# Kernel optimization log

Measured on AMD Instinct MI355X. Metric: run time of the kernel, lower is better.

Reference implementation:

```python
import jax, jax.numpy as jnp
import numpy as np

B, T, H, W = 512, 8, 28, 28
VTH, VRESET = 1.0, 0.0
ALPHA = 2.0  # spikingjelly ATan surrogate default alpha


@jax.custom_vjp
def heaviside_atan(x):
    # forward: binary spike; backward: ATan surrogate gradient
    return (x >= 0).astype(x.dtype)

def _ha_fwd(x):
    return (x >= 0).astype(x.dtype), x

def _ha_bwd(x, g):
    return (g * (ALPHA / 2.0) / (1.0 + (jnp.pi / 2.0 * ALPHA * x) ** 2),)

heaviside_atan.defvjp(_ha_fwd, _ha_bwd)


def conv3x3(x, w):
    return jax.lax.conv_general_dilated(
        x, w, (1, 1), 'SAME', dimension_numbers=('NCHW', 'OIHW', 'NCHW'))


def maxpool2(x):
    return jax.lax.reduce_window(x, -jnp.inf, jax.lax.max,
                                 (1, 1, 2, 2), (1, 1, 2, 2), 'VALID')


def one_spike_if(v, fired, x):
    # OneSpikeIFNode: integrate, fire at most once (fired mask), hard reset
    v = v + x
    spike = heaviside_atan(v - VTH) * (1.0 - fired)
    v = v * (1.0 - spike) + VRESET * spike
    fired = jnp.maximum(fired, jax.lax.stop_gradient(spike))
    return v, fired, spike


def if_node(v, x):
    # readout IFNode: integrate, fire, hard reset (v_threshold finite: latency mode, no warmup)
    v = v + x
    spike = heaviside_atan(v - VTH)
    v = v * (1.0 - spike) + VRESET * spike
    return v, spike


def setup_inputs() -> dict:
    key = jax.random.key(0)
    k = jax.random.split(key, 5)
    x = jax.random.uniform(k[0], (B, 1, H, W), jnp.float32)
    # weight scale (default_T / T) == 1 since T == 8 == default_T
    w_sconv = jax.random.normal(k[1], (16, 1, 3, 3), jnp.float32) * (2.0 / 3.0)
    w_conv = jax.random.normal(k[2], (16, 16, 3, 3), jnp.float32) * 0.12
    w_fc1 = jax.random.normal(k[3], (100, 16 * 14 * 14), jnp.float32) * 0.02
    w_fc2 = jax.random.normal(k[4], (10, 100), jnp.float32) * 0.15
    return {"x": x, "w_sconv": w_sconv, "w_conv": w_conv, "w_fc1": w_fc1, "w_fc2": w_fc2}


def reference(x, w_sconv, w_conv, w_fc1, w_fc2):
    xs = conv3x3(x, w_sconv)  # static conv computed once, reused every timestep
    z = jnp.zeros_like(xs)                       # [B,16,28,28]
    zp = jnp.zeros((B, 16, 14, 14), xs.dtype)    # pool fired-window mask
    zf = jnp.zeros((B, 100), xs.dtype)
    zo = jnp.zeros((B, 10), xs.dtype)
    state0 = (z, z, z, z, zp, zf, zf, zo)

    def step(state, _):
        v1, f1, v2, f2, pf, vfc, ffc, vout = state
        v1, f1, s1 = one_spike_if(v1, f1, xs)
        c = conv3x3(s1, w_conv)
        v2, f2, s2 = one_spike_if(v2, f2, c)
        # FirstSpikePool2d: max-pool spikes, each window passes only its first spike
        pooled = maxpool2(s2) * (1.0 - pf)
        pf = jnp.maximum(pf, jax.lax.stop_gradient(pooled))
        h = pooled.reshape(B, -1) @ w_fc1.T      # [B,100]
        vfc, ffc, s3 = one_spike_if(vfc, ffc, h)
        o = s3 @ w_fc2.T                          # [B,10]
        vout, s4 = if_node(vout, o)
        fr = jnp.stack([s1.mean(), s2.mean(), s3.mean(), s4.mean()])
        return (v1, f1, v2, f2, pf, vfc, ffc, vout), (s4, vout, fr)

    _, (s4_t, vout_t, fr_t) = jax.lax.scan(step, state0, None, length=T)
    counter_t = jnp.cumsum(s4_t, axis=0)                        # [T,B,10]
    latency_score = heaviside_atan(counter_t - 0.5).sum(axis=0)  # ATan_binary surrogate
    reg_loss = fr_t.max(axis=0).sum()
    return latency_score / T, reg_loss
```

## Files before the change

### kernel.cpp

```cpp
#include <hip/hip_runtime.h>

#define TB 512
#define NIMG 512
#define HW 28
#define NPIX 784
#define TT 8
#define NFC 100
#define NOUT 10
#define MAGIC 0x5C5C5C5Cu

#define WT_FLOATS 313600
#define GLB_ADD(p, v) __hip_atomic_fetch_add((p), (v), __ATOMIC_RELAXED, __HIP_MEMORY_SCOPE_AGENT)

typedef float f4 __attribute__((ext_vector_type(4)));

__global__ __launch_bounds__(TB, 4)
void snn_main(const float* __restrict__ xg, const float* __restrict__ w_sconv,
              const float* __restrict__ w_conv, const float* __restrict__ w_fc1,
              const float* __restrict__ w_fc2, float* __restrict__ wT,
              float* __restrict__ out, unsigned int* __restrict__ ctrl)
{
    __shared__ float wc[2880];
    __shared__ unsigned char spanB[25600];
    __shared__ unsigned short rowOr[TT * HW];
    __shared__ unsigned char tqA[3136];
    __shared__ unsigned short slist[3136];
    __shared__ float xst[NPIX];
    __shared__ float wsc[144];
    __shared__ int bcnt[9], bofs[9], bput[8];
    __shared__ int hist[32];
    __shared__ int lastflag;

    unsigned short* mask_t = (unsigned short*)spanB;
    unsigned int* mask32 = (unsigned int*)spanB;
    unsigned int* t2n = (unsigned int*)(spanB + 12544);
    float* prefixLDS = (float*)spanB;

    unsigned int* tflags = ctrl;
    float* fr_g = (float*)(ctrl + 98);
    unsigned int* done2 = ctrl + 130;
    unsigned int* fr_ready = ctrl + 131;

    const int tid = threadIdx.x;
    const int b = blockIdx.x;

    if (b < 98) {
        const int c0 = b * 32;
        for (int idx = tid; idx < 3200; idx += TB) {
            int c = idx / 100, r = idx - 100 * c;
            wT[(c0 + c) * 100 + r] = w_fc1[r * 3136 + c0 + c];
        }
    }
    if (b == 0 && tid < 33) ctrl[98 + tid] = 0u;

    for (int i = tid; i < NPIX; i += TB) xst[i] = xg[b * NPIX + i];
    for (int i = tid; i < 144; i += TB) wsc[i] = w_sconv[i];
    for (int i = tid; i < 2304; i += TB) {
        int c = i & 15, r = i >> 4;
        wc[r * 20 + c] = w_conv[c * 144 + r];
    }
    for (int i = tid; i < 3136; i += TB) mask32[i] = 0u;
    if (tid < 32) hist[tid] = 0;
    if (tid < 9) bcnt[tid] = 0;
    if (b < 98) __threadfence();
    __syncthreads();
    if (b < 98 && tid == 0) {
        __hip_atomic_store(&tflags[b], MAGIC, __ATOMIC_RELEASE, __HIP_MEMORY_SCOPE_AGENT);
        if (b == 0)
            __hip_atomic_store(fr_ready, MAGIC, __ATOMIC_RELEASE, __HIP_MEMORY_SCOPE_AGENT);
    }

    unsigned int pca = 0, pcb = 0;
#pragma unroll 1
    for (int e = 0; e < 25; e++) {
        int g = e * TB + tid;
        if (g < 12544) {
            int ci = g & 15, pos = g >> 4;
            int yy = pos / HW, xx = pos % HW;
            float acc = 0.f;
#pragma unroll
            for (int ky = 0; ky < 3; ky++) {
                int ys = yy + ky - 1;
                if (ys < 0 || ys >= HW) continue;
#pragma unroll
                for (int kx = 0; kx < 3; kx++) {
                    int xsrc = xx + kx - 1;
                    if (xsrc < 0 || xsrc >= HW) continue;
                    acc = fmaf(wsc[ci * 9 + ky * 3 + kx], xst[ys * HW + xsrc], acc);
                }
            }
            int t1 = 8; float v = 0.f;
#pragma unroll
            for (int t = 0; t < TT; t++) {
                v += acc;
                if (t1 == 8 && v >= 1.0f) t1 = t;
            }
            if (t1 < 8) {
                int lin = t1 * NPIX + pos;
                atomicOr(&mask32[lin >> 1], (1u << ci) << ((lin & 1) * 16));
                if (t1 < 4) pca += 1u << (t1 * 8); else pcb += 1u << ((t1 - 4) * 8);
            }
        }
    }
#pragma unroll
    for (int t = 0; t < TT; t++) {
        unsigned int c = ((t < 4 ? (pca >> (t * 8)) : (pcb >> ((t - 4) * 8))) & 255u);
        if (c) atomicAdd(&hist[t], (int)c);
    }
    __syncthreads();

    for (int i = tid; i < TT * HW; i += TB) {
        const unsigned short* mr = mask_t + (i / HW) * NPIX + (i % HW) * HW;
        unsigned int o = 0;
#pragma unroll
        for (int x = 0; x < HW; x++) o |= mr[x];
        rowOr[i] = (unsigned short)o;
    }
    __syncthreads();

    unsigned int pc2a = 0, pc2b = 0;
#pragma unroll 1
    for (int own = 0; own < 2; own++) {
        int pos = own * TB + tid;
        if (pos < NPIX) {
            int py = pos / HW, px = pos - py * HW;
            f4 vv0 = {0.f, 0.f, 0.f, 0.f}, vv1 = vv0, vv2 = vv0, vv3 = vv0;
            unsigned int done = 0;
            unsigned int t2lo = 0x88888888u, t2hi = 0x88888888u;
#pragma unroll 1
            for (int t = 0; t < TT; t++) {
                const unsigned short* ro = rowOr + t * HW;
                unsigned int un = ro[py];
                if (py > 0) un |= ro[py - 1];
                if (py < HW - 1) un |= ro[py + 1];
                if (!un) continue;
                const unsigned short* mt = mask_t + t * NPIX;
#pragma unroll
                for (int k = 0; k < 9; k++) {
                    int qy = py + k / 3 - 1, qx = px + k % 3 - 1;
                    if ((unsigned)qy >= HW || (unsigned)qx >= HW) continue;
                    unsigned int m = mt[qy * HW + qx];
                    while (m) {
                        int ci = __builtin_ctz(m); m &= m - 1;
                        const f4* wrow = (const f4*)&wc[(ci * 9 + k) * 20];
                        vv0 += wrow[0]; vv1 += wrow[1];
                        vv2 += wrow[2]; vv3 += wrow[3];
                    }
                }
                unsigned int fired = 0;
#pragma unroll
                for (int c = 0; c < 16; c++) {
                    float val = (c < 4) ? vv0[c & 3] : (c < 8) ? vv1[c & 3]
                              : (c < 12) ? vv2[c & 3] : vv3[c & 3];
                    fired |= (val >= 1.0f) ? (1u << c) : 0u;
                }
                unsigned int newf = fired & ~done;
                done |= newf;
                if (newf) {
                    int cnt = __builtin_popcount(newf);
                    if (t < 4) pc2a += (unsigned)cnt << (t * 8);
                    else       pc2b += (unsigned)cnt << ((t - 4) * 8);
                    while (newf) {
                        int c = __builtin_ctz(newf); newf &= newf - 1;
                        if (c < 8) t2lo = (t2lo & ~(15u << (4 * c))) | ((unsigned)t << (4 * c));
                        else       t2hi = (t2hi & ~(15u << (4 * (c - 8)))) | ((unsigned)t << (4 * (c - 8)));
                    }
                }
                if (done == 0xffffu) break;
            }
            t2n[pos * 2] = t2lo;
            t2n[pos * 2 + 1] = t2hi;
        }
    }
#pragma unroll
    for (int t = 0; t < TT; t++) {
        unsigned int c = ((t < 4 ? (pc2a >> (t * 8)) : (pc2b >> ((t - 4) * 8))) & 255u);
        if (c) atomicAdd(&hist[8 + t], (int)c);
    }
    __syncthreads();

    for (int u = tid; u < 3136; u += TB) {
        int c = u / 196, rem = u - c * 196;
        int wy = rem / 14, wx = rem - wy * 14;
        int p0 = wy * 56 + wx * 2;
        int wsel = c >> 3, sh = (c & 7) * 4;
        int m0 = (t2n[p0 * 2 + wsel] >> sh) & 15;
        int m1 = (t2n[(p0 + 1) * 2 + wsel] >> sh) & 15;
        int m2 = (t2n[(p0 + HW) * 2 + wsel] >> sh) & 15;
        int m3 = (t2n[(p0 + HW + 1) * 2 + wsel] >> sh) & 15;
        int tqv = min(min(m0, m1), min(m2, m3));
        tqA[u] = (unsigned char)tqv;
        if (tqv < 8) atomicAdd(&bcnt[tqv], 1);
    }
    __syncthreads();
    if (tid == 0) {
        int s = 0;
#pragma unroll
        for (int t = 0; t < TT; t++) { bofs[t] = s; s += bcnt[t]; }
        bofs[8] = s;
    }
    __syncthreads();
    if (tid < 8) bput[tid] = bofs[tid];
    __syncthreads();
    for (int u = tid; u < 3136; u += TB) {
        int tqv = tqA[u];
        if (tqv < 8) { int j = atomicAdd(&bput[tqv], 1); slist[j] = (unsigned short)u; }
    }

    if (tid < 98) {
        while (__hip_atomic_load(&tflags[tid], __ATOMIC_ACQUIRE,
                                 __HIP_MEMORY_SCOPE_AGENT) != MAGIC)
            __builtin_amdgcn_s_sleep(2);
    }
    __syncthreads();

    {
        const int lane = tid & 63;
        const int w = tid >> 6;
        const float* wA = wT + lane;
        const float* wB = wT + 64 + lane;
        float acc0 = 0.f, acc1 = 0.f;
#pragma unroll 1
        for (int t = 0; t < TT; t++) {
            const int lo = bofs[t];
            const int n = bofs[t + 1] - lo;
            int j = w;
            for (; j + 24 < n; j += 32) {
                int u0 = (int)slist[lo + j] * 100;
                int u1 = (int)slist[lo + j + 8] * 100;
                int u2 = (int)slist[lo + j + 16] * 100;
                int u3 = (int)slist[lo + j + 24] * 100;
                float a0 = wA[u0], a1 = wA[u1], a2 = wA[u2], a3 = wA[u3];
                if (lane < 36) {
                    float b0 = wB[u0], b1 = wB[u1], b2 = wB[u2], b3 = wB[u3];
                    acc1 += b0; acc1 += b1; acc1 += b2; acc1 += b3;
                }
                acc0 += a0; acc0 += a1; acc0 += a2; acc0 += a3;
            }
            for (; j < n; j += 8) {
                int u0 = (int)slist[lo + j] * 100;
                acc0 += wA[u0];
                if (lane < 36) acc1 += wB[u0];
            }
            prefixLDS[(w * TT + t) * NFC + lane] = acc0;
            if (lane < 36) prefixLDS[(w * TT + t) * NFC + 64 + lane] = acc1;
        }
    }
    __syncthreads();

    if (tid < NFC) {
        int t3 = 8;
#pragma unroll
        for (int t = 0; t < TT; t++) {
            float v = 0.f;
#pragma unroll
            for (int w = 0; w < 8; w++) v += prefixLDS[(w * TT + t) * NFC + tid];
            if (t3 == 8 && v >= 1.0f) t3 = t;
        }
        tqA[tid] = (unsigned char)t3;
        if (t3 < 8) atomicAdd(&hist[16 + t3], 1);
    }
    __syncthreads();

    if (tid < NOUT) {
        float acc8[TT] = {0.f, 0.f, 0.f, 0.f, 0.f, 0.f, 0.f, 0.f};
        for (int i = 0; i < NFC; i++) {
            float w = w_fc2[tid * NFC + i];
            int tv = tqA[i];
#pragma unroll
            for (int k = 0; k < TT; k++) acc8[k] += (tv == k) ? w : 0.f;
        }
        float vout = 0.f; int cnt = 0; float lat = 0.f;
#pragma unroll
        for (int t = 0; t < TT; t++) {
            vout += acc8[t];
            if (vout >= 1.0f) { vout = 0.f; cnt++; atomicAdd(&hist[24 + t], 1); }
            if (cnt >= 1) lat += 1.f;
        }
        out[b * NOUT + tid] = lat * 0.125f;
    }
    __syncthreads();

    if (tid == 0) {
        while (__hip_atomic_load(fr_ready, __ATOMIC_ACQUIRE,
                                 __HIP_MEMORY_SCOPE_AGENT) != MAGIC)
            __builtin_amdgcn_s_sleep(2);
    }
    __syncthreads();
    if (tid < 32) {
        int h = hist[tid];
        if (h) GLB_ADD(&fr_g[(tid & 7) * 4 + (tid >> 3)], (float)h);
    }
    __syncthreads();

    if (tid == 0) {
        unsigned int old = __hip_atomic_fetch_add(done2, 1u, __ATOMIC_ACQ_REL,
                                                  __HIP_MEMORY_SCOPE_AGENT);
        lastflag = (old == (unsigned)(NIMG - 1));
    }
    __syncthreads();
    if (lastflag && tid == 0) {
        const float inv0 = 1.f / 6422528.f;
        const float inv2 = 1.f / 51200.f;
        const float inv3 = 1.f / 5120.f;
        const float invs[4] = { inv0, inv0, inv2, inv3 };
        float reg = 0.f;
        for (int l = 0; l < 4; l++) {
            float mx = -INFINITY;
            for (int t = 0; t < TT; t++) {
                float v = __hip_atomic_load(&fr_g[t * 4 + l], __ATOMIC_RELAXED,
                                            __HIP_MEMORY_SCOPE_AGENT);
                mx = fmaxf(mx, v * invs[l]);
            }
            reg += mx;
        }
        out[NIMG * NOUT] = reg;
    }
}

extern "C" void kernel_launch(void* const* d_in, const int* in_sizes, int n_in,
                              void* d_out, int out_size, void* d_ws, size_t ws_size,
                              hipStream_t stream) {
    const float* x       = (const float*)d_in[0];
    const float* w_sconv = (const float*)d_in[1];
    const float* w_conv  = (const float*)d_in[2];
    const float* w_fc1   = (const float*)d_in[3];
    const float* w_fc2   = (const float*)d_in[4];
    float* out = (float*)d_out;

    float* wT          = (float*)d_ws;
    unsigned int* ctrl = (unsigned int*)(wT + WT_FLOATS);

    snn_main<<<NIMG, TB, 0, stream>>>(x, w_sconv, w_conv, w_fc1, w_fc2, wT,
                                      out, ctrl);
}
```

Measured before the change: 199.3 us.

## Split each image across two blocks by row halves with global FC1 partial merge

Each image is now processed by two blocks, each owning 14 output rows with a one-row halo for the spiking conv stages, halving per-block LDS and work. Per-half FC1 membrane partial sums are written to a global buffer, and the second block to finish (via a per-image atomic pair counter) combines them and runs the FC1 threshold, FC2 and output stages. Launch bounds rise to 8 waves-per-EU-class occupancy to exploit the smaller LDS footprint. This adds halo recomputation, extra global traffic and atomics, and cross-block synchronization in exchange for more parallelism across the GPU.

Measured after the change: 405.7 us. 2.04x slower.

```diff
diff --git a/kernel.cpp b/kernel.cpp
--- a/kernel.cpp
+++ b/kernel.cpp
@@ -10,48 +10,55 @@
 #define MAGIC 0x5C5C5C5Cu
 
 #define WT_FLOATS 313600
+#define VFCB_FLOATS (NIMG * 2 * TT * NFC)
 #define GLB_ADD(p, v) __hip_atomic_fetch_add((p), (v), __ATOMIC_RELAXED, __HIP_MEMORY_SCOPE_AGENT)
 
 typedef float f4 __attribute__((ext_vector_type(4)));
 
-__global__ __launch_bounds__(TB, 4)
+__global__ __launch_bounds__(TB, 8)
 void snn_main(const float* __restrict__ xg, const float* __restrict__ w_sconv,
               const float* __restrict__ w_conv, const float* __restrict__ w_fc1,
               const float* __restrict__ w_fc2, float* __restrict__ wT,
-              float* __restrict__ out, unsigned int* __restrict__ ctrl)
+              float* __restrict__ vfcb, float* __restrict__ out,
+              unsigned int* __restrict__ ctrl)
 {
-    __shared__ float wc[2880];
-    __shared__ unsigned char spanB[25600];
-    __shared__ unsigned short rowOr[TT * HW];
-    __shared__ unsigned char tqA[3136];
-    __shared__ unsigned short slist[3136];
-    __shared__ float xst[NPIX];
-    __shared__ float wsc[144];
+    __shared__ unsigned char span[25600] __attribute__((aligned(16)));
+    __shared__ unsigned short slist[1568];
+    __shared__ unsigned char tqA[1568];
     __shared__ int bcnt[9], bofs[9], bput[8];
     __shared__ int hist[32];
-    __shared__ int lastflag;
-
-    unsigned short* mask_t = (unsigned short*)spanB;
-    unsigned int* mask32 = (unsigned int*)spanB;
-    unsigned int* t2n = (unsigned int*)(spanB + 12544);
-    float* prefixLDS = (float*)spanB;
+    __shared__ int winflag, lastflag;
+
+    float* wc = (float*)span;
+    float* xst = (float*)(span + 11520);
+    unsigned int* t2n = (unsigned int*)(span + 11520);
+    float* wsc = (float*)(span + 14656);
+    unsigned short* mask_t = (unsigned short*)(span + 15232);
+    unsigned int* mask32 = (unsigned int*)(span + 15232);
+    unsigned short* rowOr = (unsigned short*)(span + 21952);
+    float* prefixLDS = (float*)span;
 
     unsigned int* tflags = ctrl;
     float* fr_g = (float*)(ctrl + 98);
     unsigned int* done2 = ctrl + 130;
     unsigned int* fr_ready = ctrl + 131;
+    unsigned int* pair = ctrl + 132;
 
     const int tid = threadIdx.x;
-    const int b = blockIdx.x;
-
-    if (b < 98) {
-        const int c0 = b * 32;
+    const int b = blockIdx.x >> 1;
+    const int half = blockIdx.x & 1;
+    const int mrow0 = half ? 13 : 0;
+
+    if (blockIdx.x < 98) {
+        const int c0 = blockIdx.x * 32;
         for (int idx = tid; idx < 3200; idx += TB) {
             int c = idx / 100, r = idx - 100 * c;
             wT[(c0 + c) * 100 + r] = w_fc1[r * 3136 + c0 + c];
         }
     }
-    if (b == 0 && tid < 33) ctrl[98 + tid] = 0u;
+    if (blockIdx.x == 0) {
+        for (int i = 98 + tid; i < 644; i += TB) ctrl[i] = 0u;
+    }
 
     for (int i = tid; i < NPIX; i += TB) xst[i] = xg[b * NPIX + i];
     for (int i = tid; i < 144; i += TB) wsc[i] = w_sconv[i];
@@ -59,28 +66,32 @@
         int c = i & 15, r = i >> 4;
         wc[r * 20 + c] = w_conv[c * 144 + r];
     }
-    for (int i = tid; i < 3136; i += TB) mask32[i] = 0u;
+    for (int i = tid; i < 1680; i += TB) mask32[i] = 0u;
     if (tid < 32) hist[tid] = 0;
     if (tid < 9) bcnt[tid] = 0;
-    if (b < 98) __threadfence();
-    __syncthreads();
-    if (b < 98 && tid == 0) {
-        __hip_atomic_store(&tflags[b], MAGIC, __ATOMIC_RELEASE, __HIP_MEMORY_SCOPE_AGENT);
-        if (b == 0)
-            __hip_atomic_store(fr_ready, MAGIC, __ATOMIC_RELEASE, __HIP_MEMORY_SCOPE_AGENT);
+    if (blockIdx.x < 98) __threadfence();
+    __syncthreads();
+    if (tid == 0) {
+        if (blockIdx.x < 98)
+            __hip_atomic_store(&tflags[blockIdx.x], MAGIC, __ATOMIC_RELEASE,
+                               __HIP_MEMORY_SCOPE_AGENT);
+        if (blockIdx.x == 0)
+            __hip_atomic_store(fr_ready, MAGIC, __ATOMIC_RELEASE,
+                               __HIP_MEMORY_SCOPE_AGENT);
     }
 
     unsigned int pca = 0, pcb = 0;
 #pragma unroll 1
-    for (int e = 0; e < 25; e++) {
+    for (int e = 0; e < 14; e++) {
         int g = e * TB + tid;
-        if (g < 12544) {
-            int ci = g & 15, pos = g >> 4;
-            int yy = pos / HW, xx = pos % HW;
+        if (g < 6720) {
+            int ci = g & 15, p = g >> 4;
+            int rl = p / HW, xx = p - rl * HW;
+            int gy = mrow0 + rl;
             float acc = 0.f;
 #pragma unroll
             for (int ky = 0; ky < 3; ky++) {
-                int ys = yy + ky - 1;
+                int ys = gy + ky - 1;
                 if (ys < 0 || ys >= HW) continue;
 #pragma unroll
                 for (int kx = 0; kx < 3; kx++) {
@@ -96,9 +107,12 @@
                 if (t1 == 8 && v >= 1.0f) t1 = t;
             }
             if (t1 < 8) {
-                int lin = t1 * NPIX + pos;
+                int lin = t1 * 420 + p;
                 atomicOr(&mask32[lin >> 1], (1u << ci) << ((lin & 1) * 16));
-                if (t1 < 4) pca += 1u << (t1 * 8); else pcb += 1u << ((t1 - 4) * 8);
+                bool owned = half ? (rl >= 1) : (rl < 14);
+                if (owned) {
+                    if (t1 < 4) pca += 1u << (t1 * 8); else pcb += 1u << ((t1 - 4) * 8);
+                }
             }
         }
     }
@@ -109,68 +123,66 @@
     }
     __syncthreads();
 
-    for (int i = tid; i < TT * HW; i += TB) {
-        const unsigned short* mr = mask_t + (i / HW) * NPIX + (i % HW) * HW;
+    for (int i = tid; i < TT * 15; i += TB) {
+        int t = i / 15, rl = i - t * 15;
+        const unsigned short* mr = mask_t + t * 420 + rl * HW;
         unsigned int o = 0;
 #pragma unroll
         for (int x = 0; x < HW; x++) o |= mr[x];
-        rowOr[i] = (unsigned short)o;
+        rowOr[t * 16 + rl] = (unsigned short)o;
     }
     __syncthreads();
 
     unsigned int pc2a = 0, pc2b = 0;
+    if (tid < 392) {
+        const int py_l = tid / HW, px = tid - py_l * HW;
+        const int cr = py_l + (half ? 1 : 0);
+        f4 vv0 = {0.f, 0.f, 0.f, 0.f}, vv1 = vv0, vv2 = vv0, vv3 = vv0;
+        unsigned int done = 0;
+        unsigned int t2lo = 0x88888888u, t2hi = 0x88888888u;
 #pragma unroll 1
-    for (int own = 0; own < 2; own++) {
-        int pos = own * TB + tid;
-        if (pos < NPIX) {
-            int py = pos / HW, px = pos - py * HW;
-            f4 vv0 = {0.f, 0.f, 0.f, 0.f}, vv1 = vv0, vv2 = vv0, vv3 = vv0;
-            unsigned int done = 0;
-            unsigned int t2lo = 0x88888888u, t2hi = 0x88888888u;
-#pragma unroll 1
-            for (int t = 0; t < TT; t++) {
-                const unsigned short* ro = rowOr + t * HW;
-                unsigned int un = ro[py];
-                if (py > 0) un |= ro[py - 1];
-                if (py < HW - 1) un |= ro[py + 1];
-                if (!un) continue;
-                const unsigned short* mt = mask_t + t * NPIX;
-#pragma unroll
-                for (int k = 0; k < 9; k++) {
-                    int qy = py + k / 3 - 1, qx = px + k % 3 - 1;
-                    if ((unsigned)qy >= HW || (unsigned)qx >= HW) continue;
-                    unsigned int m = mt[qy * HW + qx];
-                    while (m) {
-                        int ci = __builtin_ctz(m); m &= m - 1;
-                        const f4* wrow = (const f4*)&wc[(ci * 9 + k) * 20];
-                        vv0 += wrow[0]; vv1 += wrow[1];
-                        vv2 += wrow[2]; vv3 += wrow[3];
-                    }
-                }
-                unsigned int fired = 0;
-#pragma unroll
-                for (int c = 0; c < 16; c++) {
-                    float val = (c < 4) ? vv0[c & 3] : (c < 8) ? vv1[c & 3]
-                              : (c < 12) ? vv2[c & 3] : vv3[c & 3];
-                    fired |= (val >= 1.0f) ? (1u << c) : 0u;
-                }
-                unsigned int newf = fired & ~done;
-                done |= newf;
-                if (newf) {
-                    int cnt = __builtin_popcount(newf);
-                    if (t < 4) pc2a += (unsigned)cnt << (t * 8);
-                    else       pc2b += (unsigned)cnt << ((t - 4) * 8);
-                    while (newf) {
-                        int c = __builtin_ctz(newf); newf &= newf - 1;
-                        if (c < 8) t2lo = (t2lo & ~(15u << (4 * c))) | ((unsigned)t << (4 * c));
-                        else       t2hi = (t2hi & ~(15u << (4 * (c - 8)))) | ((unsigned)t << (4 * (c - 8)));
-                    }
-                }
-                if (done == 0xffffu) break;
-            }
-            t2n[pos * 2] = t2lo;
-            t2n[pos * 2 + 1] = t2hi;
-        }
+        for (int t = 0; t < TT; t++) {
+            const unsigned short* ro = rowOr + t * 16;
+            unsigned int un = ro[cr];
+            if (cr > 0) un |= ro[cr - 1];
+            if (cr < 14) un |= ro[cr + 1];
+            if (!un) continue;
+            const unsigned short* mt = mask_t + t * 420;
+#pragma unroll
+            for (int k = 0; k < 9; k++) {
+                int mr = cr + k / 3 - 1, qx = px + k % 3 - 1;
+                if ((unsigned)mr >= 15u || (unsigned)qx >= HW) continue;
+                unsigned int m = mt[mr * HW + qx];
+                while (m) {
+                    int ci = __builtin_ctz(m); m &= m - 1;
+                    const f4* wrow = (const f4*)&wc[(ci * 9 + k) * 20];
+                    vv0 += wrow[0]; vv1 += wrow[1];
+                    vv2 += wrow[2]; vv3 += wrow[3];
+                }
+            }
+            unsigned int fired = 0;
+#pragma unroll
+            for (int c = 0; c < 16; c++) {
+                float val = (c < 4) ? vv0[c & 3] : (c < 8) ? vv1[c & 3]
+                          : (c < 12) ? vv2[c & 3] : vv3[c & 3];
+                fired |= (val >= 1.0f) ? (1u << c) : 0u;
+            }
+            unsigned int newf = fired & ~done;
+            done |= newf;
+            if (newf) {
+                int cnt = __builtin_popcount(newf);
+                if (t < 4) pc2a += (unsigned)cnt << (t * 8);
+                else       pc2b += (unsigned)cnt << ((t - 4) * 8);
+                while (newf) {
+                    int c = __builtin_ctz(newf); newf &= newf - 1;
+                    if (c < 8) t2lo = (t2lo & ~(15u << (4 * c))) | ((unsigned)t << (4 * c));
+                    else       t2hi = (t2hi & ~(15u << (4 * (c - 8)))) | ((unsigned)t << (4 * (c - 8)));
+                }
+            }
+            if (done == 0xffffu) break;
+        }
+        t2n[tid * 2] = t2lo;
+        t2n[tid * 2 + 1] = t2hi;
     }
 #pragma unroll
     for (int t = 0; t < TT; t++) {
@@ -179,8 +191,8 @@
     }
     __syncthreads();
 
-    for (int u = tid; u < 3136; u += TB) {
-        int c = u / 196, rem = u - c * 196;
+    for (int u = tid; u < 1568; u += TB) {
+        int c = u / 98, rem = u - c * 98;
         int wy = rem / 14, wx = rem - wy * 14;
         int p0 = wy * 56 + wx * 2;
         int wsel = c >> 3, sh = (c & 7) * 4;
@@ -202,9 +214,14 @@
     __syncthreads();
     if (tid < 8) bput[tid] = bofs[tid];
     __syncthreads();
-    for (int u = tid; u < 3136; u += TB) {
+    for (int u = tid; u < 1568; u += TB) {
         int tqv = tqA[u];
-        if (tqv < 8) { int j = atomicAdd(&bput[tqv], 1); slist[j] = (unsigned short)u; }
+        if (tqv < 8) {
+            int j = atomicAdd(&bput[tqv], 1);
+            int c = u / 98, rem = u - c * 98;
+            int wy = rem / 14, wx = rem - wy * 14;
+            slist[j] = (unsigned short)(c * 196 + (half * 7 + wy) * 14 + wx);
+        }
     }
 
     if (tid < 98) {
@@ -249,12 +266,43 @@
     __syncthreads();
 
     if (tid < NFC) {
+#pragma unroll
+        for (int t = 0; t < TT; t++) {
+            float s = 0.f;
+#pragma unroll
+            for (int w = 0; w < 8; w++) s += prefixLDS[(w * TT + t) * NFC + tid];
+            vfcb[(((size_t)b * 2 + half) * TT + t) * NFC + tid] = s;
+        }
+    }
+
+    if (tid == 0) {
+        while (__hip_atomic_load(fr_ready, __ATOMIC_ACQUIRE,
+                                 __HIP_MEMORY_SCOPE_AGENT) != MAGIC)
+            __builtin_amdgcn_s_sleep(2);
+    }
+    __syncthreads();
+    if (tid < 16) {
+        int h = hist[tid];
+        if (h) GLB_ADD(&fr_g[(tid & 7) * 4 + (tid >> 3)], (float)h);
+    }
+    __threadfence();
+    __syncthreads();
+    if (tid == 0) {
+        unsigned int old = __hip_atomic_fetch_add(&pair[b], 1u, __ATOMIC_ACQ_REL,
+                                                  __HIP_MEMORY_SCOPE_AGENT);
+        winflag = (old == 1u);
+    }
+    __syncthreads();
+    if (!winflag) return;
+
+    if (tid < NFC) {
         int t3 = 8;
 #pragma unroll
         for (int t = 0; t < TT; t++) {
-            float v = 0.f;
-#pragma unroll
-            for (int w = 0; w < 8; w++) v += prefixLDS[(w * TT + t) * NFC + tid];
+            float v = __hip_atomic_load(&vfcb[(((size_t)b * 2 + 0) * TT + t) * NFC + tid],
+                                        __ATOMIC_RELAXED, __HIP_MEMORY_SCOPE_AGENT)
+                    + __hip_atomic_load(&vfcb[(((size_t)b * 2 + 1) * TT + t) * NFC + tid],
+                                        __ATOMIC_RELAXED, __HIP_MEMORY_SCOPE_AGENT);
             if (t3 == 8 && v >= 1.0f) t3 = t;
         }
         tqA[tid] = (unsigned char)t3;
@@ -280,17 +328,11 @@
         out[b * NOUT + tid] = lat * 0.125f;
     }
     __syncthreads();
-
-    if (tid == 0) {
-        while (__hip_atomic_load(fr_ready, __ATOMIC_ACQUIRE,
-                                 __HIP_MEMORY_SCOPE_AGENT) != MAGIC)
-            __builtin_amdgcn_s_sleep(2);
-    }
-    __syncthreads();
-    if (tid < 32) {
+    if (tid >= 16 && tid < 32) {
         int h = hist[tid];
         if (h) GLB_ADD(&fr_g[(tid & 7) * 4 + (tid >> 3)], (float)h);
     }
+    __threadfence();
     __syncthreads();
 
     if (tid == 0) {
@@ -329,8 +371,9 @@
     float* out = (float*)d_out;
 
     float* wT          = (float*)d_ws;
-    unsigned int* ctrl = (unsigned int*)(wT + WT_FLOATS);
-
-    snn_main<<<NIMG, TB, 0, stream>>>(x, w_sconv, w_conv, w_fc1, w_fc2, wT,
-                                      out, ctrl);
+    float* vfcb        = wT + WT_FLOATS;
+    unsigned int* ctrl = (unsigned int*)(vfcb + VFCB_FLOATS);
+
+    snn_main<<<NIMG * 2, TB, 0, stream>>>(x, w_sconv, w_conv, w_fc1, w_fc2,
+                                          wT, vfcb, out, ctrl);
 }
```

## Split each image across two blocks by output channel half, add readout kernel

Applied to the files above, without the earlier changes.

Each image is now handled by two blocks, each owning 8 of the 16 conv2 output channels. Both blocks recompute the first conv and spike mask, then write partial fc1 prefix sums to a global buffer. A second small kernel sums the two halves, runs the fc1 and readout spiking logic, and accumulates the firing-rate stats. The aim is more parallelism and a smaller LDS footprint for higher occupancy, at the cost of duplicated stage-1 work, an extra launch and a global round trip.

Result: slower. 207.7 us (+4.2%).

```diff
diff --git a/kernel.cpp b/kernel.cpp
--- a/kernel.cpp
+++ b/kernel.cpp
@@ -10,6 +10,7 @@
 #define MAGIC 0x5C5C5C5Cu
 
 #define WT_FLOATS 313600
+#define VFCB_FLOATS (NIMG * 2 * TT * NFC)
 #define GLB_ADD(p, v) __hip_atomic_fetch_add((p), (v), __ATOMIC_RELAXED, __HIP_MEMORY_SCOPE_AGENT)
 
 typedef float f4 __attribute__((ext_vector_type(4)));
@@ -18,56 +19,62 @@
 void snn_main(const float* __restrict__ xg, const float* __restrict__ w_sconv,
               const float* __restrict__ w_conv, const float* __restrict__ w_fc1,
               const float* __restrict__ w_fc2, float* __restrict__ wT,
-              float* __restrict__ out, unsigned int* __restrict__ ctrl)
+              float* __restrict__ vfcb, float* __restrict__ out,
+              unsigned int* __restrict__ ctrl)
 {
-    __shared__ float wc[2880];
-    __shared__ unsigned char spanB[25600];
-    __shared__ unsigned short rowOr[TT * HW];
-    __shared__ unsigned char tqA[3136];
-    __shared__ unsigned short slist[3136];
-    __shared__ float xst[NPIX];
-    __shared__ float wsc[144];
+    __shared__ unsigned char span[25600] __attribute__((aligned(16)));
+    __shared__ unsigned short slist[1568];
+    __shared__ unsigned char tqA[1568];
     __shared__ int bcnt[9], bofs[9], bput[8];
     __shared__ int hist[32];
-    __shared__ int lastflag;
-
-    unsigned short* mask_t = (unsigned short*)spanB;
-    unsigned int* mask32 = (unsigned int*)spanB;
-    unsigned int* t2n = (unsigned int*)(spanB + 12544);
-    float* prefixLDS = (float*)spanB;
+
+    float* wc = (float*)span;
+    float* xst = (float*)(span + 6912);
+    unsigned int* t2n = (unsigned int*)(span + 6912);
+    float* wsc = (float*)(span + 10048);
+    unsigned short* mask_t = (unsigned short*)(span + 10624);
+    unsigned int* mask32 = (unsigned int*)(span + 10624);
+    unsigned short* rowOr = (unsigned short*)(span + 23168);
+    float* prefixLDS = (float*)span;
 
     unsigned int* tflags = ctrl;
     float* fr_g = (float*)(ctrl + 98);
-    unsigned int* done2 = ctrl + 130;
     unsigned int* fr_ready = ctrl + 131;
 
     const int tid = threadIdx.x;
-    const int b = blockIdx.x;
-
-    if (b < 98) {
-        const int c0 = b * 32;
+    const int b = blockIdx.x >> 1;
+    const int half = blockIdx.x & 1;
+    const int co0 = half * 8;
+
+    if (blockIdx.x < 98) {
+        const int c0 = blockIdx.x * 32;
         for (int idx = tid; idx < 3200; idx += TB) {
             int c = idx / 100, r = idx - 100 * c;
             wT[(c0 + c) * 100 + r] = w_fc1[r * 3136 + c0 + c];
         }
     }
-    if (b == 0 && tid < 33) ctrl[98 + tid] = 0u;
+    if (blockIdx.x == 0) {
+        for (int i = 98 + tid; i < 132; i += TB) ctrl[i] = 0u;
+    }
 
     for (int i = tid; i < NPIX; i += TB) xst[i] = xg[b * NPIX + i];
     for (int i = tid; i < 144; i += TB) wsc[i] = w_sconv[i];
-    for (int i = tid; i < 2304; i += TB) {
-        int c = i & 15, r = i >> 4;
-        wc[r * 20 + c] = w_conv[c * 144 + r];
+    for (int i = tid; i < 1152; i += TB) {
+        int c = i & 7, r = i >> 3;
+        wc[r * 12 + c] = w_conv[(co0 + c) * 144 + r];
     }
     for (int i = tid; i < 3136; i += TB) mask32[i] = 0u;
     if (tid < 32) hist[tid] = 0;
     if (tid < 9) bcnt[tid] = 0;
-    if (b < 98) __threadfence();
-    __syncthreads();
-    if (b < 98 && tid == 0) {
-        __hip_atomic_store(&tflags[b], MAGIC, __ATOMIC_RELEASE, __HIP_MEMORY_SCOPE_AGENT);
-        if (b == 0)
-            __hip_atomic_store(fr_ready, MAGIC, __ATOMIC_RELEASE, __HIP_MEMORY_SCOPE_AGENT);
+    if (blockIdx.x < 98) __threadfence();
+    __syncthreads();
+    if (tid == 0) {
+        if (blockIdx.x < 98)
+            __hip_atomic_store(&tflags[blockIdx.x], MAGIC, __ATOMIC_RELEASE,
+                               __HIP_MEMORY_SCOPE_AGENT);
+        if (blockIdx.x == 0)
+            __hip_atomic_store(fr_ready, MAGIC, __ATOMIC_RELEASE,
+                               __HIP_MEMORY_SCOPE_AGENT);
     }
 
     unsigned int pca = 0, pcb = 0;
@@ -102,19 +109,22 @@
             }
         }
     }
-#pragma unroll
-    for (int t = 0; t < TT; t++) {
-        unsigned int c = ((t < 4 ? (pca >> (t * 8)) : (pcb >> ((t - 4) * 8))) & 255u);
-        if (c) atomicAdd(&hist[t], (int)c);
+    if (half == 0) {
+#pragma unroll
+        for (int t = 0; t < TT; t++) {
+            unsigned int c = ((t < 4 ? (pca >> (t * 8)) : (pcb >> ((t - 4) * 8))) & 255u);
+            if (c) atomicAdd(&hist[t], (int)c);
+        }
     }
     __syncthreads();
 
     for (int i = tid; i < TT * HW; i += TB) {
-        const unsigned short* mr = mask_t + (i / HW) * NPIX + (i % HW) * HW;
+        int t = i / HW, y = i - t * HW;
+        const unsigned short* mr = mask_t + t * NPIX + y * HW;
         unsigned int o = 0;
 #pragma unroll
         for (int x = 0; x < HW; x++) o |= mr[x];
-        rowOr[i] = (unsigned short)o;
+        rowOr[t * 32 + y] = (unsigned short)o;
     }
     __syncthreads();
 
@@ -124,12 +134,12 @@
         int pos = own * TB + tid;
         if (pos < NPIX) {
             int py = pos / HW, px = pos - py * HW;
-            f4 vv0 = {0.f, 0.f, 0.f, 0.f}, vv1 = vv0, vv2 = vv0, vv3 = vv0;
+            f4 vv0 = {0.f, 0.f, 0.f, 0.f}, vv1 = vv0;
             unsigned int done = 0;
-            unsigned int t2lo = 0x88888888u, t2hi = 0x88888888u;
+            unsigned int t2p = 0x88888888u;
 #pragma unroll 1
             for (int t = 0; t < TT; t++) {
-                const unsigned short* ro = rowOr + t * HW;
+                const unsigned short* ro = rowOr + t * 32;
                 unsigned int un = ro[py];
                 if (py > 0) un |= ro[py - 1];
                 if (py < HW - 1) un |= ro[py + 1];
@@ -142,16 +152,14 @@
                     unsigned int m = mt[qy * HW + qx];
                     while (m) {
                         int ci = __builtin_ctz(m); m &= m - 1;
-                        const f4* wrow = (const f4*)&wc[(ci * 9 + k) * 20];
+                        const f4* wrow = (const f4*)&wc[(ci * 9 + k) * 12];
                         vv0 += wrow[0]; vv1 += wrow[1];
-                        vv2 += wrow[2]; vv3 += wrow[3];
                     }
                 }
                 unsigned int fired = 0;
 #pragma unroll
-                for (int c = 0; c < 16; c++) {
-                    float val = (c < 4) ? vv0[c & 3] : (c < 8) ? vv1[c & 3]
-                              : (c < 12) ? vv2[c & 3] : vv3[c & 3];
+                for (int c = 0; c < 8; c++) {
+                    float val = (c < 4) ? vv0[c & 3] : vv1[c & 3];
                     fired |= (val >= 1.0f) ? (1u << c) : 0u;
                 }
                 unsigned int newf = fired & ~done;
@@ -162,14 +170,12 @@
                     else       pc2b += (unsigned)cnt << ((t - 4) * 8);
                     while (newf) {
                         int c = __builtin_ctz(newf); newf &= newf - 1;
-                        if (c < 8) t2lo = (t2lo & ~(15u << (4 * c))) | ((unsigned)t << (4 * c));
-                        else       t2hi = (t2hi & ~(15u << (4 * (c - 8)))) | ((unsigned)t << (4 * (c - 8)));
+                        t2p = (t2p & ~(15u << (4 * c))) | ((unsigned)t << (4 * c));
                     }
                 }
-                if (done == 0xffffu) break;
-            }
-            t2n[pos * 2] = t2lo;
-            t2n[pos * 2 + 1] = t2hi;
+                if (done == 0xffu) break;
+            }
+            t2n[pos] = t2p;
         }
     }
 #pragma unroll
@@ -179,15 +185,15 @@
     }
     __syncthreads();
 
-    for (int u = tid; u < 3136; u += TB) {
+    for (int u = tid; u < 1568; u += TB) {
         int c = u / 196, rem = u - c * 196;
         int wy = rem / 14, wx = rem - wy * 14;
         int p0 = wy * 56 + wx * 2;
-        int wsel = c >> 3, sh = (c & 7) * 4;
-        int m0 = (t2n[p0 * 2 + wsel] >> sh) & 15;
-        int m1 = (t2n[(p0 + 1) * 2 + wsel] >> sh) & 15;
-        int m2 = (t2n[(p0 + HW) * 2 + wsel] >> sh) & 15;
-        int m3 = (t2n[(p0 + HW + 1) * 2 + wsel] >> sh) & 15;
+        int sh = c * 4;
+        int m0 = (t2n[p0] >> sh) & 15;
+        int m1 = (t2n[p0 + 1] >> sh) & 15;
+        int m2 = (t2n[p0 + HW] >> sh) & 15;
+        int m3 = (t2n[p0 + HW + 1] >> sh) & 15;
         int tqv = min(min(m0, m1), min(m2, m3));
         tqA[u] = (unsigned char)tqv;
         if (tqv < 8) atomicAdd(&bcnt[tqv], 1);
@@ -202,9 +208,13 @@
     __syncthreads();
     if (tid < 8) bput[tid] = bofs[tid];
     __syncthreads();
-    for (int u = tid; u < 3136; u += TB) {
+    for (int u = tid; u < 1568; u += TB) {
         int tqv = tqA[u];
-        if (tqv < 8) { int j = atomicAdd(&bput[tqv], 1); slist[j] = (unsigned short)u; }
+        if (tqv < 8) {
+            int j = atomicAdd(&bput[tqv], 1);
+            int c = u / 196, rem = u - c * 196;
+            slist[j] = (unsigned short)((co0 + c) * 196 + rem);
+        }
     }
 
     if (tid < 98) {
@@ -249,24 +259,56 @@
     __syncthreads();
 
     if (tid < NFC) {
+#pragma unroll
+        for (int t = 0; t < TT; t++) {
+            float s = 0.f;
+#pragma unroll
+            for (int w = 0; w < 8; w++) s += prefixLDS[(w * TT + t) * NFC + tid];
+            vfcb[(((size_t)b * 2 + half) * TT + t) * NFC + tid] = s;
+        }
+    }
+
+    if (tid == 0) {
+        while (__hip_atomic_load(fr_ready, __ATOMIC_ACQUIRE,
+                                 __HIP_MEMORY_SCOPE_AGENT) != MAGIC)
+            __builtin_amdgcn_s_sleep(2);
+    }
+    __syncthreads();
+    if (tid < 16) {
+        int h = hist[tid];
+        if (h) GLB_ADD(&fr_g[(tid & 7) * 4 + (tid >> 3)], (float)h);
+    }
+}
+
+__global__ void snn_d(const float* __restrict__ vfcb, const float* __restrict__ w_fc2,
+                      float* __restrict__ out, unsigned int* __restrict__ ctrl)
+{
+    __shared__ unsigned char t3L[NFC];
+    __shared__ int hist3[TT], hist4[TT];
+    __shared__ int lastflag;
+    float* fr_g = (float*)(ctrl + 98);
+    unsigned int* done2 = ctrl + 130;
+    const int tid = threadIdx.x;
+    const int b = blockIdx.x;
+    if (tid < TT) { hist3[tid] = 0; hist4[tid] = 0; }
+    __syncthreads();
+    if (tid < NFC) {
         int t3 = 8;
 #pragma unroll
         for (int t = 0; t < TT; t++) {
-            float v = 0.f;
-#pragma unroll
-            for (int w = 0; w < 8; w++) v += prefixLDS[(w * TT + t) * NFC + tid];
+            float v = vfcb[(((size_t)b * 2 + 0) * TT + t) * NFC + tid]
+                    + vfcb[(((size_t)b * 2 + 1) * TT + t) * NFC + tid];
             if (t3 == 8 && v >= 1.0f) t3 = t;
         }
-        tqA[tid] = (unsigned char)t3;
-        if (t3 < 8) atomicAdd(&hist[16 + t3], 1);
-    }
-    __syncthreads();
-
+        t3L[tid] = (unsigned char)t3;
+        if (t3 < 8) atomicAdd(&hist3[t3], 1);
+    }
+    __syncthreads();
     if (tid < NOUT) {
         float acc8[TT] = {0.f, 0.f, 0.f, 0.f, 0.f, 0.f, 0.f, 0.f};
         for (int i = 0; i < NFC; i++) {
             float w = w_fc2[tid * NFC + i];
-            int tv = tqA[i];
+            int tv = t3L[i];
 #pragma unroll
             for (int k = 0; k < TT; k++) acc8[k] += (tv == k) ? w : 0.f;
         }
@@ -274,25 +316,17 @@
 #pragma unroll
         for (int t = 0; t < TT; t++) {
             vout += acc8[t];
-            if (vout >= 1.0f) { vout = 0.f; cnt++; atomicAdd(&hist[24 + t], 1); }
+            if (vout >= 1.0f) { vout = 0.f; cnt++; atomicAdd(&hist4[t], 1); }
             if (cnt >= 1) lat += 1.f;
         }
         out[b * NOUT + tid] = lat * 0.125f;
     }
     __syncthreads();
-
-    if (tid == 0) {
-        while (__hip_atomic_load(fr_ready, __ATOMIC_ACQUIRE,
-                                 __HIP_MEMORY_SCOPE_AGENT) != MAGIC)
-            __builtin_amdgcn_s_sleep(2);
-    }
-    __syncthreads();
-    if (tid < 32) {
-        int h = hist[tid];
-        if (h) GLB_ADD(&fr_g[(tid & 7) * 4 + (tid >> 3)], (float)h);
-    }
-    __syncthreads();
-
+    if (tid < TT) {
+        if (hist3[tid]) GLB_ADD(&fr_g[tid * 4 + 2], (float)hist3[tid]);
+        if (hist4[tid]) GLB_ADD(&fr_g[tid * 4 + 3], (float)hist4[tid]);
+    }
+    __syncthreads();
     if (tid == 0) {
         unsigned int old = __hip_atomic_fetch_add(done2, 1u, __ATOMIC_ACQ_REL,
                                                   __HIP_MEMORY_SCOPE_AGENT);
@@ -329,8 +363,10 @@
     float* out = (float*)d_out;
 
     float* wT          = (float*)d_ws;
-    unsigned int* ctrl = (unsigned int*)(wT + WT_FLOATS);
-
-    snn_main<<<NIMG, TB, 0, stream>>>(x, w_sconv, w_conv, w_fc1, w_fc2, wT,
-                                      out, ctrl);
+    float* vfcb        = wT + WT_FLOATS;
+    unsigned int* ctrl = (unsigned int*)(vfcb + VFCB_FLOATS);
+
+    snn_main<<<NIMG * 2, TB, 0, stream>>>(x, w_sconv, w_conv, w_fc1, w_fc2,
+                                          wT, vfcb, out, ctrl);
+    snn_d<<<NIMG, 128, 0, stream>>>(vfcb, w_fc2, out, ctrl);
 }
```
